# Performance work log

Hardware: AMD Instinct MI355X
Metric: run time of the kernel (lower is better)

## Reference

```python
import jax, jax.numpy as jnp
import numpy as np

N_QUBITS = 10
N_LAYERS = 2
B = 4096
D_IN = 512
D_OUT = 256


def _apply_1q(state, gate, wire, n):
    # state: (B, 2**n) complex64; gate: (2,2) shared or (B,2,2) batched
    b = state.shape[0]
    left, right = 2 ** wire, 2 ** (n - wire - 1)
    s = state.reshape(b, left, 2, right)
    if gate.ndim == 3:
        s = jnp.einsum('bij,bljr->blir', gate, s)
    else:
        s = jnp.einsum('ij,bljr->blir', gate, s)
    return s.reshape(b, 2 ** n)


def _apply_cnot(state, c, t, n):
    # CNOT(control=c, target=t): flip target axis on the control=1 slice
    b = state.shape[0]
    a, d = (c, t) if c < t else (t, c)
    s = state.reshape(b, 2 ** a, 2, 2 ** (d - a - 1), 2, 2 ** (n - d - 1))
    if c < t:
        s = s.at[:, :, 1].set(jnp.flip(s[:, :, 1], axis=3))
    else:
        s = s.at[:, :, :, :, 1].set(jnp.flip(s[:, :, :, :, 1], axis=2))
    return s.reshape(b, 2 ** n)


def _quantum_circuit(angles, qweights):
    # AngleEmbedding (RX) + StronglyEntanglingLayers (Rot + ring CNOTs), expval(PauliZ_i)
    b, n = angles.shape
    n_layers = qweights.shape[0]
    state = jnp.zeros((b, 2 ** n), jnp.complex64).at[:, 0].set(1.0)
    # AngleEmbedding default rotation='X': RX(angle_i) on wire i
    half = 0.5 * angles
    cx = jnp.cos(half).astype(jnp.complex64)
    sx = ((-1j) * jnp.sin(half)).astype(jnp.complex64)
    for i in range(n):
        gate = jnp.stack([jnp.stack([cx[:, i], sx[:, i]], -1),
                          jnp.stack([sx[:, i], cx[:, i]], -1)], -2)  # (B,2,2)
        state = _apply_1q(state, gate, i, n)
    for l in range(n_layers):
        phi, theta, omega = qweights[l, :, 0], qweights[l, :, 1], qweights[l, :, 2]
        ct = jnp.cos(0.5 * theta).astype(jnp.complex64)
        st = jnp.sin(0.5 * theta).astype(jnp.complex64)
        epo = jnp.exp(-0.5j * (phi + omega)).astype(jnp.complex64)
        epm = jnp.exp(-0.5j * (phi - omega)).astype(jnp.complex64)
        # Rot(phi,theta,omega) = RZ(omega) RY(theta) RZ(phi)
        gates = jnp.stack([jnp.stack([epo * ct, -jnp.conj(epm) * st], -1),
                           jnp.stack([epm * st, jnp.conj(epo) * ct], -1)], -2)  # (n,2,2)
        for i in range(n):
            state = _apply_1q(state, gates[i], i, n)
        if n > 1:
            r = (l % (n - 1)) + 1  # default StronglyEntanglingLayers range
            for i in range(n):
                state = _apply_cnot(state, i, (i + r) % n, n)
    probs = state.real ** 2 + state.imag ** 2  # (B, 2**n)
    k = np.arange(2 ** n)
    # wire 0 is the most-significant bit; z_i = +1 for bit 0, -1 for bit 1
    zmat = (1 - 2 * ((k[None, :] >> (n - 1 - np.arange(n))[:, None]) & 1)).astype(np.float32)
    return probs @ zmat.T  # (B, n)


def setup_inputs() -> dict:
    key = jax.random.key(0)
    ks = jax.random.split(key, 6)
    x = jax.random.normal(ks[0], (B, D_IN), jnp.float32)
    W_in = jax.random.normal(ks[1], (D_IN, N_QUBITS), jnp.float32) / np.float32(np.sqrt(D_IN))
    b_in = jnp.zeros((N_QUBITS,), jnp.float32)
    qweights = jax.random.uniform(ks[2], (N_LAYERS, N_QUBITS, 3), jnp.float32, 0.0, 2.0 * np.pi)
    W1 = jax.random.normal(ks[3], (N_QUBITS, 64), jnp.float32) / np.float32(np.sqrt(N_QUBITS))
    b1 = jnp.zeros((64,), jnp.float32)
    W2 = jax.random.normal(ks[4], (64, D_OUT), jnp.float32) / np.float32(8.0)
    b2 = jnp.zeros((D_OUT,), jnp.float32)
    return {'x': x, 'W_in': W_in, 'b_in': b_in, 'qweights': qweights,
            'W1': W1, 'b1': b1, 'W2': W2, 'b2': b2}


def reference(x, W_in, b_in, qweights, W1, b1, W2, b2):
    angles = x @ W_in + b_in          # input projection -> rotation angles
    z = _quantum_circuit(angles, qweights)  # (B, n_qubits) PauliZ expvals
    h = jax.nn.relu(z @ W1 + b1)
    return jnp.tanh(h @ W2 + b2)
```

## Files before the change

kernel.cpp:

```cpp
#include <hip/hip_runtime.h>
#include <math.h>

#define NQ 10

__device__ __forceinline__ void write_term(int u, const float abc[NQ][3],
                                           uint2* __restrict__ terms) {
    const int lane = u & 255, s = u >> 8;
    const int wvv = lane >> 6;
    const int nsl = (wvv == 0) ? 8 : ((wvv == 3) ? 4 : 3);
    int q = -1, g0 = 0;
    if      (lane < 32)  { q = 8; g0 = 0;   }
    else if (lane < 64)  { q = 9; g0 = 32;  }
    else if (lane < 96)  { q = 0; g0 = 64;  }
    else if (lane < 128) { q = 1; g0 = 96;  }
    else if (lane < 160) { q = 6; g0 = 128; }
    else if (lane < 192) { q = 7; g0 = 160; }
    else if (lane < 200) { q = 4; g0 = 192; }
    else if (lane < 208) { q = 5; g0 = 200; }
    else if (lane < 216) { q = 2; g0 = 208; }
    else if (lane < 224) { q = 3; g0 = 216; }
    if (q < 0 || s >= nsl) { terms[u] = make_uint2(0u, 0u); return; }
    const int tau = (lane - g0) * nsl + s;

    int m = 1 << q;
    for (int ii = NQ - 1; ii >= 0; --ii) {
        int tt = (ii + 2) % NQ;
        if ((m >> tt) & 1) m ^= 1 << ii;
    }
    const int Lp = __popc(m);
    int cnt = 1;
    for (int k = 0; k < Lp; ++k) cnt *= 3;
    if (tau >= cnt) { terms[u] = make_uint2(0u, 0u); return; }

    int rem = tau;
    unsigned xm = 0, zm = 0;
    float coef = 1.f;
    for (int i = 0; i < NQ; ++i) {
        if ((m >> i) & 1) {
            int d = rem % 3; rem /= 3;
            coef *= abc[i][d];
            if (d == 0)      { xm |= 1u << i; }
            else if (d == 1) { xm |= 1u << i; zm |= 1u << i; }
            else             { zm |= 1u << i; }
        }
    }
    unsigned sgn = 0;
    for (int i = NQ - 1; i >= 0; --i) {
        int c = i, tt = (i + 1) % NQ;
        unsigned xc = (xm >> c) & 1u, zt = (zm >> tt) & 1u;
        unsigned xt = (xm >> tt) & 1u, zc = (zm >> c) & 1u;
        sgn ^= xc & zt & (xt ^ zc ^ 1u);
        xm ^= xc << tt;
        zm ^= zt << c;
    }
    if (sgn) coef = -coef;

    unsigned w = 0;
    for (int i = 0; i < NQ; ++i) {
        unsigned code = ((xm >> i) & 1u) | (((zm >> i) & 1u) << 1);
        w |= code << (2 * i);
    }
    terms[u] = make_uint2(w, __float_as_uint(coef));
}

__global__ __launch_bounds__(256) void qse_setup(const float* __restrict__ qw,
                                                 uint2* __restrict__ terms,
                                                 float* __restrict__ Rmat) {
    __shared__ float abc[NQ][3];
    const int t = threadIdx.x;
    const int b = blockIdx.x;
    if (t < NQ) {
        if (b == 0) {
            float phi = qw[t * 3 + 0], th = qw[t * 3 + 1], om = qw[t * 3 + 2];
            float st_, ct;  sincosf(0.5f * th, &st_, &ct);
            float spo, cpo; sincosf(0.5f * (phi + om), &spo, &cpo);
            float spm, cpm; sincosf(0.5f * (phi - om), &spm, &cpm);
            Rmat[t * 8 + 0] =  cpo * ct;  Rmat[t * 8 + 1] = -spo * ct;
            Rmat[t * 8 + 2] = -cpm * st_; Rmat[t * 8 + 3] = -spm * st_;
            Rmat[t * 8 + 4] =  cpm * st_; Rmat[t * 8 + 5] = -spm * st_;
            Rmat[t * 8 + 6] =  cpo * ct;  Rmat[t * 8 + 7] =  spo * ct;
        }
        {
            float phi = qw[30 + t * 3 + 0], th = qw[30 + t * 3 + 1], om = qw[30 + t * 3 + 2];
            float st_, ct;  sincosf(0.5f * th, &st_, &ct);
            float spo, cpo; sincosf(0.5f * (phi + om), &spo, &cpo);
            float spm, cpm; sincosf(0.5f * (phi - om), &spm, &cpm);
            float2 G00 = make_float2(cpo * ct, -spo * ct);
            float2 G01 = make_float2(-cpm * st_, -spm * st_);
            float2 G10 = make_float2(cpm * st_, -spm * st_);
            float2 G11 = make_float2(cpo * ct, spo * ct);
            float re = G00.x * G01.x + G00.y * G01.y - (G10.x * G11.x + G10.y * G11.y);
            float im = G00.x * G01.y - G00.y * G01.x - (G10.x * G11.y - G10.y * G11.x);
            float A00 = G00.x * G00.x + G00.y * G00.y - (G10.x * G10.x + G10.y * G10.y);
            float A11 = G01.x * G01.x + G01.y * G01.y - (G11.x * G11.x + G11.y * G11.y);
            abc[t][0] = re;
            abc[t][1] = -im;
            abc[t][2] = 0.5f * (A00 - A11);
        }
    }
    __syncthreads();
    write_term(b * 256 + t, abc, terms);
}

__device__ __forceinline__ float fast_tanh(float v) {
    float e = __expf(2.f * v);
    return 1.f - 2.f / (e + 1.f);
}

__global__ __launch_bounds__(256) void qse_mega(
    const float* __restrict__ x,
    const float* __restrict__ W_in,
    const float* __restrict__ b_in,
    const float* __restrict__ W1,
    const float* __restrict__ b1,
    const float* __restrict__ W2,
    const float* __restrict__ b2,
    const uint2* __restrict__ terms,
    const float* __restrict__ Rmat,
    float* __restrict__ out)
{
    __shared__ float angsh[4][NQ];
    __shared__ float E2tmp[4][5][16];
    __shared__ float E4d[4][2][256];
    __shared__ float E2P[4][32];
    __shared__ float zsh[4][NQ];
    __shared__ float hsh[4][64];

    const int t = threadIdx.x;
    const int lane = t & 63;
    const int wv = t >> 6;
    const int row0 = blockIdx.x * 4;
    const int nsl = (wv == 0) ? 8 : ((wv == 3) ? 4 : 3);

    uint2 tm[8];
    #pragma unroll
    for (int s = 0; s < 8; ++s)
        tm[s] = (s < nsl) ? terms[s * 256 + t] : make_uint2(0u, 0u);

    {
        float acc[NQ];
        #pragma unroll
        for (int q = 0; q < NQ; ++q) acc[q] = 0.f;
        const float4* xr4 = (const float4*)(x + (size_t)(row0 + wv) * 512);
        #pragma unroll
        for (int k = 0; k < 2; ++k) {
            const int j4 = lane + 64 * k;
            const float4 xv = xr4[j4];
            const float* wr = W_in + (4 * j4) * NQ;
            #pragma unroll
            for (int h = 0; h < 5; ++h) {
                float2 w2 = ((const float2*)wr)[h];
                acc[2*h]   = fmaf(xv.x, w2.x, acc[2*h]);
                acc[2*h+1] = fmaf(xv.x, w2.y, acc[2*h+1]);
            }
            #pragma unroll
            for (int h = 0; h < 5; ++h) {
                float2 w2 = ((const float2*)(wr + NQ))[h];
                acc[2*h]   = fmaf(xv.y, w2.x, acc[2*h]);
                acc[2*h+1] = fmaf(xv.y, w2.y, acc[2*h+1]);
            }
            #pragma unroll
            for (int h = 0; h < 5; ++h) {
                float2 w2 = ((const float2*)(wr + 2 * NQ))[h];
                acc[2*h]   = fmaf(xv.z, w2.x, acc[2*h]);
                acc[2*h+1] = fmaf(xv.z, w2.y, acc[2*h+1]);
            }
            #pragma unroll
            for (int h = 0; h < 5; ++h) {
                float2 w2 = ((const float2*)(wr + 3 * NQ))[h];
                acc[2*h]   = fmaf(xv.w, w2.x, acc[2*h]);
                acc[2*h+1] = fmaf(xv.w, w2.y, acc[2*h+1]);
            }
        }
        #pragma unroll
        for (int off = 32; off > 0; off >>= 1) {
            #pragma unroll
            for (int q = 0; q < NQ; ++q) acc[q] += __shfl_xor(acc[q], off);
        }
        if (lane == 0) {
            #pragma unroll
            for (int q = 0; q < NQ; ++q) angsh[wv][q] = acc[q] + b_in[q];
        }
    }
    __syncthreads();

    if (t < 80) {
        const int rr = t / 20, rem = t % 20, p = rem >> 2, c1 = rem & 3;
        const int i0 = 2 * p, i1 = i0 + 1;
        float a0 = angsh[rr][i0];
        float a1 = angsh[rr][i1];
        float s0, c0f, s1, c1f;
        sincosf(0.5f * a0, &s0, &c0f);
        sincosf(0.5f * a1, &s1, &c1f);
        const float* Rp0 = Rmat + i0 * 8;
        const float* Rp1 = Rmat + i1 * 8;
        float2 u0 = make_float2(fmaf(Rp0[0], c0f, s0 * Rp0[3]), fmaf(Rp0[1], c0f, -s0 * Rp0[2]));
        float2 u1 = make_float2(fmaf(Rp0[4], c0f, s0 * Rp0[7]), fmaf(Rp0[5], c0f, -s0 * Rp0[6]));
        float ex0 = 2.f * (u0.x * u1.x + u0.y * u1.y);
        float ey0 = 2.f * (u0.x * u1.y - u0.y * u1.x);
        float ez0 = u0.x * u0.x + u0.y * u0.y - u1.x * u1.x - u1.y * u1.y;
        float2 v0 = make_float2(fmaf(Rp1[0], c1f, s1 * Rp1[3]), fmaf(Rp1[1], c1f, -s1 * Rp1[2]));
        float2 v1 = make_float2(fmaf(Rp1[4], c1f, s1 * Rp1[7]), fmaf(Rp1[5], c1f, -s1 * Rp1[6]));
        float ex1 = 2.f * (v0.x * v1.x + v0.y * v1.y);
        float ey1 = 2.f * (v0.x * v1.y - v0.y * v1.x);
        float ez1 = v0.x * v0.x + v0.y * v0.y - v1.x * v1.x - v1.y * v1.y;
        float e1 = (c1 == 0) ? 1.f : (c1 == 1) ? ex1 : (c1 == 2) ? ez1 : ey1;
        float e0arr[4] = {1.f, ex0, ez0, ey0};
        #pragma unroll
        for (int cc = 0; cc < 4; ++cc) {
            float v = e0arr[cc] * e1;
            int idx = cc | (c1 << 2);
            E2tmp[rr][p][idx] = v;
            if (p == 4) {
                E2P[rr][2 * idx]     = v;
                E2P[rr][2 * idx + 1] = v;
            }
        }
    }
    __syncthreads();

    #pragma unroll
    for (int k = 0; k < 8; ++k) {
        const int rr = k >> 1, qd = k & 1;
        E4d[rr][qd][t] = E2tmp[rr][2 * qd][t & 15] * E2tmp[rr][2 * qd + 1][t >> 4];
    }
    __syncthreads();

    float accR[4] = {0.f, 0.f, 0.f, 0.f};
    {
        const int par = t & 1;
        #pragma unroll
        for (int s = 0; s < 8; ++s) {
            if (s < nsl) {
                const float cf = __uint_as_float(tm[s].y);
                const unsigned w = tm[s].x;
                const int i0 = w & 255, i1 = (w >> 8) & 255, ip = (w >> 16) & 15;
                #pragma unroll
                for (int rr = 0; rr < 4; ++rr) {
                    float pr = cf * E4d[rr][0][i0];
                    pr *= E4d[rr][1][i1];
                    pr *= E2P[rr][2 * ip + par];
                    accR[rr] += pr;
                }
            }
        }
    }
    #pragma unroll
    for (int rr = 0; rr < 4; ++rr) {
        accR[rr] += __shfl_xor(accR[rr], 1);
        accR[rr] += __shfl_xor(accR[rr], 2);
        accR[rr] += __shfl_xor(accR[rr], 4);
    }
    if (t < 192) {
        #pragma unroll
        for (int rr = 0; rr < 4; ++rr) {
            accR[rr] += __shfl_xor(accR[rr], 8);
            accR[rr] += __shfl_xor(accR[rr], 16);
        }
    }
    {
        int qx = -1;
        if      (t == 0)   qx = 8;
        else if (t == 32)  qx = 9;
        else if (t == 64)  qx = 0;
        else if (t == 96)  qx = 1;
        else if (t == 128) qx = 6;
        else if (t == 160) qx = 7;
        else if (t == 192) qx = 4;
        else if (t == 200) qx = 5;
        else if (t == 208) qx = 2;
        else if (t == 216) qx = 3;
        if (qx >= 0) {
            #pragma unroll
            for (int rr = 0; rr < 4; ++rr) zsh[rr][qx] = accR[rr];
        }
    }
    __syncthreads();

    {
        const int rr = t >> 6, c = t & 63;
        float a = b1[c];
        #pragma unroll
        for (int i = 0; i < NQ; ++i) a = fmaf(zsh[rr][i], W1[i * 64 + c], a);
        hsh[rr][c] = fmaxf(a, 0.f);
    }
    __syncthreads();

    {
        float oacc[4];
        const float bb = b2[t];
        #pragma unroll
        for (int rr = 0; rr < 4; ++rr) oacc[rr] = bb;
        for (int j4 = 0; j4 < 16; ++j4) {
            const float w0 = W2[(4 * j4 + 0) * 256 + t];
            const float w1 = W2[(4 * j4 + 1) * 256 + t];
            const float w2 = W2[(4 * j4 + 2) * 256 + t];
            const float w3 = W2[(4 * j4 + 3) * 256 + t];
            #pragma unroll
            for (int rr = 0; rr < 4; ++rr) {
                float4 hv = *(const float4*)&hsh[rr][4 * j4];
                oacc[rr] = fmaf(hv.x, w0, oacc[rr]);
                oacc[rr] = fmaf(hv.y, w1, oacc[rr]);
                oacc[rr] = fmaf(hv.z, w2, oacc[rr]);
                oacc[rr] = fmaf(hv.w, w3, oacc[rr]);
            }
        }
        #pragma unroll
        for (int rr = 0; rr < 4; ++rr)
            out[(size_t)(row0 + rr) * 256 + t] = fast_tanh(oacc[rr]);
    }
}

extern "C" void kernel_launch(void* const* d_in, const int* in_sizes, int n_in,
                              void* d_out, int out_size, void* d_ws, size_t ws_size,
                              hipStream_t stream) {
    const float* x    = (const float*)d_in[0];
    const float* W_in = (const float*)d_in[1];
    const float* b_in = (const float*)d_in[2];
    const float* qw   = (const float*)d_in[3];
    const float* W1   = (const float*)d_in[4];
    const float* b1   = (const float*)d_in[5];
    const float* W2   = (const float*)d_in[6];
    const float* b2   = (const float*)d_in[7];
    float* out = (float*)d_out;

    uint2* terms = (uint2*)d_ws;
    float* Rmat  = (float*)((char*)d_ws + 16384);

    qse_setup<<<8, 256, 0, stream>>>(qw, terms, Rmat);
    qse_mega<<<1024, 256, 0, stream>>>(x, W_in, b_in, W1, b1, W2, b2,
                                       (const uint2*)terms, (const float*)Rmat, out);
}
```

Measured before the change: 84.92 us.

## Fuse setup into main kernel with compile-time Pauli term table

Removes the separate setup kernel launch. The Pauli term structure (masks and CNOT sign) is now built at compile time as a device constexpr table, and the weight-dependent coefficients are rebuilt inside every block from shared-memory tables via the same factorized product trick. W_in is also staged transposed in shared memory so the projection reads it from LDS instead of global memory. This trades one launch and its dependency gap for redundant per-block trig and table construction, about 20KB more shared memory per block, and an extra barrier.

```diff
diff --git a/kernel.cpp b/kernel.cpp
--- a/kernel.cpp
+++ b/kernel.cpp
@@ -3,82 +3,142 @@
 
 #define NQ 10
 
-__device__ __forceinline__ void write_term(int u, const float abc[NQ][3],
-                                           uint2* __restrict__ terms) {
-    const int lane = u & 255, s = u >> 8;
-    const int wvv = lane >> 6;
-    const int nsl = (wvv == 0) ? 8 : ((wvv == 3) ? 4 : 3);
-    int q = -1, g0 = 0;
-    if      (lane < 32)  { q = 8; g0 = 0;   }
-    else if (lane < 64)  { q = 9; g0 = 32;  }
-    else if (lane < 96)  { q = 0; g0 = 64;  }
-    else if (lane < 128) { q = 1; g0 = 96;  }
-    else if (lane < 160) { q = 6; g0 = 128; }
-    else if (lane < 192) { q = 7; g0 = 160; }
-    else if (lane < 200) { q = 4; g0 = 192; }
-    else if (lane < 208) { q = 5; g0 = 200; }
-    else if (lane < 216) { q = 2; g0 = 208; }
-    else if (lane < 224) { q = 3; g0 = 216; }
-    if (q < 0 || s >= nsl) { terms[u] = make_uint2(0u, 0u); return; }
-    const int tau = (lane - g0) * nsl + s;
-
-    int m = 1 << q;
-    for (int ii = NQ - 1; ii >= 0; --ii) {
-        int tt = (ii + 2) % NQ;
-        if ((m >> tt) & 1) m ^= 1 << ii;
-    }
-    const int Lp = __popc(m);
-    int cnt = 1;
-    for (int k = 0; k < Lp; ++k) cnt *= 3;
-    if (tau >= cnt) { terms[u] = make_uint2(0u, 0u); return; }
-
-    int rem = tau;
-    unsigned xm = 0, zm = 0;
-    float coef = 1.f;
-    for (int i = 0; i < NQ; ++i) {
-        if ((m >> i) & 1) {
-            int d = rem % 3; rem /= 3;
-            coef *= abc[i][d];
-            if (d == 0)      { xm |= 1u << i; }
-            else if (d == 1) { xm |= 1u << i; zm |= 1u << i; }
-            else             { zm |= 1u << i; }
-        }
-    }
-    unsigned sgn = 0;
-    for (int i = NQ - 1; i >= 0; --i) {
-        int c = i, tt = (i + 1) % NQ;
-        unsigned xc = (xm >> c) & 1u, zt = (zm >> tt) & 1u;
-        unsigned xt = (xm >> tt) & 1u, zc = (zm >> c) & 1u;
-        sgn ^= xc & zt & (xt ^ zc ^ 1u);
-        xm ^= xc << tt;
-        zm ^= zt << c;
-    }
-    if (sgn) coef = -coef;
-
-    unsigned w = 0;
-    for (int i = 0; i < NQ; ++i) {
-        unsigned code = ((xm >> i) & 1u) | (((zm >> i) & 1u) << 1);
-        w |= code << (2 * i);
-    }
-    terms[u] = make_uint2(w, __float_as_uint(coef));
+struct TP { unsigned post, pre; };
+struct TermsTab { TP t[2048]; };
+
+constexpr TermsTab build_terms() {
+    TermsTab T{};
+    for (int u = 0; u < 2048; ++u) {
+        const int lane = u & 255, s = u >> 8;
+        const int wvv = lane >> 6;
+        const int nsl = (wvv == 0) ? 8 : ((wvv == 3) ? 4 : 3);
+        int q = -1, g0 = 0;
+        if      (lane < 32)  { q = 8; g0 = 0;   }
+        else if (lane < 64)  { q = 9; g0 = 32;  }
+        else if (lane < 96)  { q = 0; g0 = 64;  }
+        else if (lane < 128) { q = 1; g0 = 96;  }
+        else if (lane < 160) { q = 6; g0 = 128; }
+        else if (lane < 192) { q = 7; g0 = 160; }
+        else if (lane < 200) { q = 4; g0 = 192; }
+        else if (lane < 208) { q = 5; g0 = 200; }
+        else if (lane < 216) { q = 2; g0 = 208; }
+        else if (lane < 224) { q = 3; g0 = 216; }
+        T.t[u].post = 0u; T.t[u].pre = 0u;
+        if (q < 0 || s >= nsl) continue;
+        const int tau = (lane - g0) * nsl + s;
+
+        int m = 1 << q;
+        for (int ii = 9; ii >= 0; --ii) {
+            int tt = (ii + 2) % 10;
+            if ((m >> tt) & 1) m ^= 1 << ii;
+        }
+        int Lp = 0;
+        for (int i = 0; i < 10; ++i) Lp += (m >> i) & 1;
+        int cnt = 1;
+        for (int k = 0; k < Lp; ++k) cnt *= 3;
+        if (tau >= cnt) continue;
+
+        int rem = tau;
+        unsigned xm = 0, zm = 0;
+        for (int i = 0; i < 10; ++i) {
+            if ((m >> i) & 1) {
+                int d = rem % 3; rem /= 3;
+                if (d == 0)      { xm |= 1u << i; }
+                else if (d == 1) { xm |= 1u << i; zm |= 1u << i; }
+                else             { zm |= 1u << i; }
+            }
+        }
+        unsigned wpre = 0;
+        for (int i = 0; i < 10; ++i)
+            wpre |= (((xm >> i) & 1u) | (((zm >> i) & 1u) << 1)) << (2 * i);
+
+        unsigned sgn = 0;
+        for (int i = 9; i >= 0; --i) {
+            int c = i, tt = (i + 1) % 10;
+            unsigned xc = (xm >> c) & 1u, zt = (zm >> tt) & 1u;
+            unsigned xt = (xm >> tt) & 1u, zc = (zm >> c) & 1u;
+            sgn ^= xc & zt & (xt ^ zc ^ 1u);
+            xm ^= xc << tt;
+            zm ^= zt << c;
+        }
+        unsigned wpost = 0;
+        for (int i = 0; i < 10; ++i)
+            wpost |= (((xm >> i) & 1u) | (((zm >> i) & 1u) << 1)) << (2 * i);
+
+        T.t[u].post = wpost;
+        T.t[u].pre  = wpre | (sgn << 20) | (1u << 21);
+    }
+    return T;
 }
 
-__global__ __launch_bounds__(256) void qse_setup(const float* __restrict__ qw,
-                                                 uint2* __restrict__ terms,
-                                                 float* __restrict__ Rmat) {
-    __shared__ float abc[NQ][3];
+__device__ constexpr TermsTab TERMS = build_terms();
+
+__device__ __forceinline__ float fast_tanh(float v) {
+    float e = __expf(2.f * v);
+    return 1.f - 2.f / (e + 1.f);
+}
+
+__global__ __launch_bounds__(256) void qse_mega(
+    const float* __restrict__ x,
+    const float* __restrict__ W_in,
+    const float* __restrict__ b_in,
+    const float* __restrict__ qw,
+    const float* __restrict__ W1,
+    const float* __restrict__ b1,
+    const float* __restrict__ W2,
+    const float* __restrict__ b2,
+    float* __restrict__ out)
+{
+    __shared__ float Wt[NQ][512];
+    __shared__ float Rsh[NQ][8];
+    __shared__ float absh[NQ][3];
+    __shared__ float angsh[4][NQ];
+    __shared__ float E2tmp[4][5][16];
+    __shared__ float E4d[4][2][256];
+    __shared__ float E2P[4][32];
+    __shared__ float A2tmp[5][16];
+    __shared__ float A4d[2][256];
+    __shared__ float A2P[32];
+    __shared__ float zsh[4][NQ];
+    __shared__ float hsh[4][64];
+
     const int t = threadIdx.x;
-    const int b = blockIdx.x;
+    const int lane = t & 63;
+    const int wv = t >> 6;
+    const int row0 = blockIdx.x * 4;
+    const int nsl = (wv == 0) ? 8 : ((wv == 3) ? 4 : 3);
+
+    const float* xr = x + (size_t)(row0 + wv) * 512;
+    float xv[8];
+    #pragma unroll
+    for (int k = 0; k < 8; ++k) xv[k] = xr[lane + 64 * k];
+
+    TP tp[8];
+    #pragma unroll
+    for (int s = 0; s < 8; ++s)
+        tp[s] = (s < nsl) ? TERMS.t[s * 256 + t] : TP{0u, 0u};
+
+    #pragma unroll
+    for (int i = 0; i < 5; ++i) {
+        const int e4 = t + 256 * i;
+        const float4 v = ((const float4*)W_in)[e4];
+        const int e = 4 * e4;
+        Wt[(e + 0) % NQ][(e + 0) / NQ] = v.x;
+        Wt[(e + 1) % NQ][(e + 1) / NQ] = v.y;
+        Wt[(e + 2) % NQ][(e + 2) / NQ] = v.z;
+        Wt[(e + 3) % NQ][(e + 3) / NQ] = v.w;
+    }
+
     if (t < NQ) {
-        if (b == 0) {
+        {
             float phi = qw[t * 3 + 0], th = qw[t * 3 + 1], om = qw[t * 3 + 2];
             float st_, ct;  sincosf(0.5f * th, &st_, &ct);
             float spo, cpo; sincosf(0.5f * (phi + om), &spo, &cpo);
             float spm, cpm; sincosf(0.5f * (phi - om), &spm, &cpm);
-            Rmat[t * 8 + 0] =  cpo * ct;  Rmat[t * 8 + 1] = -spo * ct;
-            Rmat[t * 8 + 2] = -cpm * st_; Rmat[t * 8 + 3] = -spm * st_;
-            Rmat[t * 8 + 4] =  cpm * st_; Rmat[t * 8 + 5] = -spm * st_;
-            Rmat[t * 8 + 6] =  cpo * ct;  Rmat[t * 8 + 7] =  spo * ct;
+            Rsh[t][0] =  cpo * ct;  Rsh[t][1] = -spo * ct;
+            Rsh[t][2] = -cpm * st_; Rsh[t][3] = -spm * st_;
+            Rsh[t][4] =  cpm * st_; Rsh[t][5] = -spm * st_;
+            Rsh[t][6] =  cpo * ct;  Rsh[t][7] =  spo * ct;
         }
         {
             float phi = qw[30 + t * 3 + 0], th = qw[30 + t * 3 + 1], om = qw[30 + t * 3 + 2];
@@ -93,84 +153,23 @@
             float im = G00.x * G01.y - G00.y * G01.x - (G10.x * G11.y - G10.y * G11.x);
             float A00 = G00.x * G00.x + G00.y * G00.y - (G10.x * G10.x + G10.y * G10.y);
             float A11 = G01.x * G01.x + G01.y * G01.y - (G11.x * G11.x + G11.y * G11.y);
-            abc[t][0] = re;
-            abc[t][1] = -im;
-            abc[t][2] = 0.5f * (A00 - A11);
-        }
-    }
-    __syncthreads();
-    write_term(b * 256 + t, abc, terms);
-}
-
-__device__ __forceinline__ float fast_tanh(float v) {
-    float e = __expf(2.f * v);
-    return 1.f - 2.f / (e + 1.f);
-}
-
-__global__ __launch_bounds__(256) void qse_mega(
-    const float* __restrict__ x,
-    const float* __restrict__ W_in,
-    const float* __restrict__ b_in,
-    const float* __restrict__ W1,
-    const float* __restrict__ b1,
-    const float* __restrict__ W2,
-    const float* __restrict__ b2,
-    const uint2* __restrict__ terms,
-    const float* __restrict__ Rmat,
-    float* __restrict__ out)
-{
-    __shared__ float angsh[4][NQ];
-    __shared__ float E2tmp[4][5][16];
-    __shared__ float E4d[4][2][256];
-    __shared__ float E2P[4][32];
-    __shared__ float zsh[4][NQ];
-    __shared__ float hsh[4][64];
-
-    const int t = threadIdx.x;
-    const int lane = t & 63;
-    const int wv = t >> 6;
-    const int row0 = blockIdx.x * 4;
-    const int nsl = (wv == 0) ? 8 : ((wv == 3) ? 4 : 3);
-
-    uint2 tm[8];
-    #pragma unroll
-    for (int s = 0; s < 8; ++s)
-        tm[s] = (s < nsl) ? terms[s * 256 + t] : make_uint2(0u, 0u);
+            absh[t][0] = re;
+            absh[t][1] = -im;
+            absh[t][2] = 0.5f * (A00 - A11);
+        }
+    }
+    __syncthreads();
 
     {
         float acc[NQ];
         #pragma unroll
         for (int q = 0; q < NQ; ++q) acc[q] = 0.f;
-        const float4* xr4 = (const float4*)(x + (size_t)(row0 + wv) * 512);
-        #pragma unroll
-        for (int k = 0; k < 2; ++k) {
-            const int j4 = lane + 64 * k;
-            const float4 xv = xr4[j4];
-            const float* wr = W_in + (4 * j4) * NQ;
-            #pragma unroll
-            for (int h = 0; h < 5; ++h) {
-                float2 w2 = ((const float2*)wr)[h];
-                acc[2*h]   = fmaf(xv.x, w2.x, acc[2*h]);
-                acc[2*h+1] = fmaf(xv.x, w2.y, acc[2*h+1]);
-            }
-            #pragma unroll
-            for (int h = 0; h < 5; ++h) {
-                float2 w2 = ((const float2*)(wr + NQ))[h];
-                acc[2*h]   = fmaf(xv.y, w2.x, acc[2*h]);
-                acc[2*h+1] = fmaf(xv.y, w2.y, acc[2*h+1]);
-            }
-            #pragma unroll
-            for (int h = 0; h < 5; ++h) {
-                float2 w2 = ((const float2*)(wr + 2 * NQ))[h];
-                acc[2*h]   = fmaf(xv.z, w2.x, acc[2*h]);
-                acc[2*h+1] = fmaf(xv.z, w2.y, acc[2*h+1]);
-            }
-            #pragma unroll
-            for (int h = 0; h < 5; ++h) {
-                float2 w2 = ((const float2*)(wr + 3 * NQ))[h];
-                acc[2*h]   = fmaf(xv.w, w2.x, acc[2*h]);
-                acc[2*h+1] = fmaf(xv.w, w2.y, acc[2*h+1]);
-            }
+        #pragma unroll
+        for (int k = 0; k < 8; ++k) {
+            const int j = lane + 64 * k;
+            const float xj = xv[k];
+            #pragma unroll
+            for (int q = 0; q < NQ; ++q) acc[q] = fmaf(xj, Wt[q][j], acc[q]);
         }
         #pragma unroll
         for (int off = 32; off > 0; off >>= 1) {
@@ -192,8 +191,8 @@
         float s0, c0f, s1, c1f;
         sincosf(0.5f * a0, &s0, &c0f);
         sincosf(0.5f * a1, &s1, &c1f);
-        const float* Rp0 = Rmat + i0 * 8;
-        const float* Rp1 = Rmat + i1 * 8;
+        const float* Rp0 = Rsh[i0];
+        const float* Rp1 = Rsh[i1];
         float2 u0 = make_float2(fmaf(Rp0[0], c0f, s0 * Rp0[3]), fmaf(Rp0[1], c0f, -s0 * Rp0[2]));
         float2 u1 = make_float2(fmaf(Rp0[4], c0f, s0 * Rp0[7]), fmaf(Rp0[5], c0f, -s0 * Rp0[6]));
         float ex0 = 2.f * (u0.x * u1.x + u0.y * u1.y);
@@ -216,6 +215,21 @@
                 E2P[rr][2 * idx + 1] = v;
             }
         }
+    } else if (t < 100) {
+        const int rem = t - 80, p = rem >> 2, c1 = rem & 3;
+        const int i0 = 2 * p, i1 = i0 + 1;
+        float b1v = (c1 == 0) ? 1.f : (c1 == 1) ? absh[i1][0] : (c1 == 2) ? absh[i1][2] : absh[i1][1];
+        float a0arr[4] = {1.f, absh[i0][0], absh[i0][2], absh[i0][1]};
+        #pragma unroll
+        for (int cc = 0; cc < 4; ++cc) {
+            float v = a0arr[cc] * b1v;
+            int idx = cc | (c1 << 2);
+            A2tmp[p][idx] = v;
+            if (p == 4) {
+                A2P[2 * idx]     = v;
+                A2P[2 * idx + 1] = v;
+            }
+        }
     }
     __syncthreads();
 
@@ -224,6 +238,8 @@
         const int rr = k >> 1, qd = k & 1;
         E4d[rr][qd][t] = E2tmp[rr][2 * qd][t & 15] * E2tmp[rr][2 * qd + 1][t >> 4];
     }
+    A4d[0][t] = A2tmp[0][t & 15] * A2tmp[1][t >> 4];
+    A4d[1][t] = A2tmp[2][t & 15] * A2tmp[3][t >> 4];
     __syncthreads();
 
     float accR[4] = {0.f, 0.f, 0.f, 0.f};
@@ -232,9 +248,12 @@
         #pragma unroll
         for (int s = 0; s < 8; ++s) {
             if (s < nsl) {
-                const float cf = __uint_as_float(tm[s].y);
-                const unsigned w = tm[s].x;
-                const int i0 = w & 255, i1 = (w >> 8) & 255, ip = (w >> 16) & 15;
+                const unsigned pre = tp[s].pre, post = tp[s].post;
+                float cf = A4d[0][pre & 255] * A4d[1][(pre >> 8) & 255]
+                         * A2P[2 * ((pre >> 16) & 15) + par];
+                cf = (pre & (1u << 21)) ? cf : 0.f;
+                cf = (pre & (1u << 20)) ? -cf : cf;
+                const int i0 = post & 255, i1 = (post >> 8) & 255, ip = (post >> 16) & 15;
                 #pragma unroll
                 for (int rr = 0; rr < 4; ++rr) {
                     float pr = cf * E4d[rr][0][i0];
@@ -324,10 +343,5 @@
     const float* b2   = (const float*)d_in[7];
     float* out = (float*)d_out;
 
-    uint2* terms = (uint2*)d_ws;
-    float* Rmat  = (float*)((char*)d_ws + 16384);
-
-    qse_setup<<<8, 256, 0, stream>>>(qw, terms, Rmat);
-    qse_mega<<<1024, 256, 0, stream>>>(x, W_in, b_in, W1, b1, W2, b2,
-                                       (const uint2*)terms, (const float*)Rmat, out);
+    qse_mega<<<1024, 256, 0, stream>>>(x, W_in, b_in, qw, W1, b1, W2, b2, out);
 }
```

Result: no change. 83.75 us (median of 2 runs) (-1.4%).
